# Kernel tuning notes

Hardware: AMD Instinct MI355X
Metric: run time of the kernel (lower is better)

## Reference

```python
import jax, jax.numpy as jnp
import numpy as np

N, E, B, F, D, H, M = 50000, 800000, 1, 64, 64, 4, 8
d = D // H  # head feats = 16


def setup_inputs() -> dict:
    key = jax.random.key(0)
    ks = jax.random.split(key, 16)
    s = 0.02  # init stddev, per reset_parameters
    return {
        "x_src": jax.random.normal(ks[0], (N, B, F), jnp.float32),
        "x_dst": jax.random.normal(ks[1], (N, B, F), jnp.float32),
        "t": jax.random.uniform(ks[2], (N, B, 1), jnp.float32),
        "m": jax.random.uniform(ks[3], (N, 1, M), jnp.float32),
        "ef": jax.random.normal(ks[4], (E, 1), jnp.float32),
        "Wq": s * jax.random.normal(ks[5], (D, F), jnp.float32),
        "Wk": s * jax.random.normal(ks[6], (D, F), jnp.float32),
        "Wv": s * jax.random.normal(ks[7], (D, F), jnp.float32),
        "Wt": s * jax.random.normal(ks[8], (D, F), jnp.float32),
        "We": s * jax.random.normal(ks[9], (D, 1), jnp.float32),
        "Wi": s * jax.random.normal(ks[10], (d * M, d + 1), jnp.float32),
        "bi": jnp.zeros((d * M,), jnp.float32),
        "weight_i": jax.random.normal(ks[11], (M, d), jnp.float32) / np.float32(np.sqrt(d)),
        "scale_i": jnp.zeros((M,), jnp.float32),
        "src": jax.random.randint(ks[12], (E,), 0, N, dtype=jnp.int32),
        "dst": jax.random.randint(ks[13], (E,), 0, N, dtype=jnp.int32),
    }


def reference(x_src, x_dst, t, m, ef, Wq, Wk, Wv, Wt, We, Wi, bi, weight_i, scale_i, src, dst):
    def heads(x, W):  # [N,B,F] -> [N,B,H,d]
        return (x @ W.T).reshape(x.shape[0], B, H, d)

    Q, K = heads(x_dst, Wq), heads(x_src, Wk)
    T, V = heads(x_src, Wt), heads(x_src, Wv)
    Ef = (ef @ We.T).reshape(E, 1, H, d)  # [E,1,H,d], broadcasts over batch

    # --- edge attention scores + edge_softmax over incoming edges of each dst ---
    e = jnp.sum((K[src] + Ef) * Q[dst], axis=-1) / np.float32(np.sqrt(d))  # [E,B,H]
    emax = jax.ops.segment_max(e, dst, num_segments=N)                     # [N,B,H]
    ea = jnp.exp(e - emax[dst])
    ea = ea / jax.ops.segment_sum(ea, dst, num_segments=N)[dst]            # [E,B,H]

    # --- first aggregation: attention-weighted sum of T ---
    g = jax.ops.segment_sum(T[src] * ea[..., None], dst, num_segments=N)   # [N,B,H,d]

    # --- Hawkes mark intensities ---
    tb = jnp.broadcast_to(t[:, :, None, :], (N, B, H, 1))
    u = jax.nn.sigmoid(jnp.concatenate([g, tb], axis=-1) @ Wi.T + bi)      # [N,B,H,M*d]
    u = u.reshape(N, B, H, M, d)
    scale = jnp.exp(scale_i)                                               # [M]
    z = jnp.einsum('nbhmd,md->nbhm', u, weight_i) / scale
    fi = scale * jnp.log1p(jnp.exp(z))                                     # [N,B,H,M]

    # --- intensity-gated second aggregation of V ---
    fm = m[:, :, None, :]                                                  # [N,1,1,M]
    ee = jnp.sum(fi[src] * fm[dst], axis=-1) * ea                          # [E,B,H]
    out = jax.ops.segment_sum(V[src] * ee[..., None], dst, num_segments=N) # [N,B,H,d]
    out = out.reshape(N, B, D)
    return out + x_dst  # residual
```

## Files before the change

### kernel.cpp

```cpp
#include <hip/hip_runtime.h>
#include <cmath>


__device__ __forceinline__ float softplus_f(float z){
  return fmaxf(z, 0.f) + log1pf(__expf(-fabsf(z)));
}

__global__ __launch_bounds__(256) void k_proj(
    const float* __restrict__ x_src, const float* __restrict__ x_dst,
    const float* __restrict__ Wq, const float* __restrict__ Wk,
    const float* __restrict__ Wt, const float* __restrict__ Wv,
    const float* __restrict__ We,
    float* __restrict__ Qo, float* __restrict__ Ko,
    float* __restrict__ To, float* __restrict__ Vo,
    float* __restrict__ WeQ, int N)
{
  __shared__ float sW[4*4096];
  int tid = threadIdx.x;
  {
    float4* dW = (float4*)sW;
    const float4* s0 = (const float4*)Wq;
    const float4* s1 = (const float4*)Wk;
    const float4* s2 = (const float4*)Wt;
    const float4* s3 = (const float4*)Wv;
    #pragma unroll
    for (int i=tid; i<1024; i+=256) dW[i]      = s0[i];
    #pragma unroll
    for (int i=tid; i<1024; i+=256) dW[1024+i] = s1[i];
    #pragma unroll
    for (int i=tid; i<1024; i+=256) dW[2048+i] = s2[i];
    #pragma unroll
    for (int i=tid; i<1024; i+=256) dW[3072+i] = s3[i];
  }
  __syncthreads();

  int l   = tid & 63;
  int mat = __builtin_amdgcn_readfirstlane(tid >> 6);
  int n   = blockIdx.x * 64 + l;
  if (n < N){
    const float* x = ((mat==0) ? x_dst : x_src) + (size_t)n*64;
    float*       O = (mat==0) ? Qo : (mat==1) ? Ko : (mat==2) ? To : Vo;
    const float4* Wm4 = (const float4*)(sW + (mat<<12));
    const float4* We4 = (const float4*)We;

    float xr[64];
    const float4* x4 = (const float4*)x;
    #pragma unroll
    for (int i=0;i<16;i++){ float4 v=x4[i]; xr[4*i]=v.x; xr[4*i+1]=v.y; xr[4*i+2]=v.z; xr[4*i+3]=v.w; }

    float4* O4 = (float4*)(O + (size_t)n*64);
    float weq0=0.f, weq1=0.f, weq2=0.f, weq3=0.f;
    #pragma unroll
    for (int jq=0;jq<16;jq++){
      float a0=0.f,a1=0.f,a2=0.f,a3=0.f;
      const float4* Wr4 = Wm4 + jq*64;
      #pragma unroll
      for (int f4=0;f4<16;f4++){
        float4 w0 = Wr4[f4], w1 = Wr4[16+f4], w2 = Wr4[32+f4], w3 = Wr4[48+f4];
        float x0=xr[4*f4], x1=xr[4*f4+1], x2=xr[4*f4+2], x3=xr[4*f4+3];
        a0=fmaf(w0.x,x0,a0); a0=fmaf(w0.y,x1,a0); a0=fmaf(w0.z,x2,a0); a0=fmaf(w0.w,x3,a0);
        a1=fmaf(w1.x,x0,a1); a1=fmaf(w1.y,x1,a1); a1=fmaf(w1.z,x2,a1); a1=fmaf(w1.w,x3,a1);
        a2=fmaf(w2.x,x0,a2); a2=fmaf(w2.y,x1,a2); a2=fmaf(w2.z,x2,a2); a2=fmaf(w2.w,x3,a2);
        a3=fmaf(w3.x,x0,a3); a3=fmaf(w3.y,x1,a3); a3=fmaf(w3.z,x2,a3); a3=fmaf(w3.w,x3,a3);
      }
      O4[jq] = make_float4(a0,a1,a2,a3);
      if (mat==0){
        float4 we = We4[jq];
        float ws = we.x*a0 + we.y*a1 + we.z*a2 + we.w*a3;
        if      (jq <  4) weq0 += ws;
        else if (jq <  8) weq1 += ws;
        else if (jq < 12) weq2 += ws;
        else              weq3 += ws;
      }
    }
    if (mat==0) *(float4*)(WeQ + (size_t)n*4) = make_float4(weq0,weq1,weq2,weq3);
  }
}

__global__ __launch_bounds__(256) void k_hist(const int* __restrict__ dst, int* __restrict__ deg, int E){
  int i = blockIdx.x*256 + threadIdx.x;
  if (i < E) atomicAdd(&deg[dst[i]], 1);
}

__global__ __launch_bounds__(1024) void k_scan1(const int* __restrict__ deg, int* __restrict__ rowptr,
                                                int* __restrict__ bsum, int N){
  __shared__ int sh[1024];
  int t = threadIdx.x;
  int i = blockIdx.x*1024 + t;
  int v = (i < N) ? deg[i] : 0;
  sh[t] = v; __syncthreads();
  int x = v;
  for (int off=1; off<1024; off<<=1){
    int y = (t >= off) ? sh[t-off] : 0;
    __syncthreads();
    x += y; sh[t] = x;
    __syncthreads();
  }
  if (i < N) rowptr[i] = x - v;
  if (t == 1023) bsum[blockIdx.x] = x;
}

__global__ __launch_bounds__(64) void k_scan2(int* __restrict__ bsum, int nb){
  int l = threadIdx.x;
  int v0 = (l < nb) ? bsum[l] : 0;
  int v = v0;
  for (int off=1; off<64; off<<=1){
    int y = __shfl_up(v, off);
    if (l >= off) v += y;
  }
  if (l < nb) bsum[l] = v - v0;
}

__global__ __launch_bounds__(1024) void k_scan3(int* __restrict__ rowptr, const int* __restrict__ bsum,
                                                int N, int E){
  int i = blockIdx.x*1024 + threadIdx.x;
  if (i < N) rowptr[i] += bsum[blockIdx.x];
  if (i == 0) rowptr[N] = E;
}

__global__ __launch_bounds__(256) void k_scatter(const int* __restrict__ dst, const int* __restrict__ src,
                                                 const float* __restrict__ ef,
                                                 const int* __restrict__ rowptr,
                                                 int* __restrict__ fill,
                                                 int2* __restrict__ sedge, int E){
  int i = blockIdx.x*256 + threadIdx.x;
  if (i < E){
    int d_ = dst[i];
    int pos = rowptr[d_] + atomicAdd(&fill[d_], 1);
    sedge[pos] = make_int2(src[i], __float_as_int(ef[i]));
  }
}

__global__ __launch_bounds__(256) void k_node(
    const float* __restrict__ Qb, const float* __restrict__ Kb, const float* __restrict__ Tb,
    const float* __restrict__ WeQ, const float* __restrict__ t_in,
    const int* __restrict__ rowptr, const int2* __restrict__ sedge,
    const float* __restrict__ Wi, const float* __restrict__ bi,
    const float* __restrict__ wiw, const float* __restrict__ scale_i,
    float* __restrict__ es, float* __restrict__ esum,
    float* __restrict__ fi_out, int N)
{
  __shared__ float sWi[128*17];
  __shared__ float sbi[128];
  __shared__ float swiw[128];
  __shared__ float sscale[8];
  __shared__ float g_sh[4][4][17];
  __shared__ float tr[4][64][9];
  int tid = threadIdx.x;
  for (int i=tid; i<128*17; i+=256) sWi[i] = Wi[i];
  if (tid < 128){ sbi[tid] = bi[tid]; swiw[tid] = wiw[tid]; }
  if (tid < 8)  sscale[tid] = __expf(scale_i[tid]);
  __syncthreads();

  int w = tid>>6, l = tid&63;
  int h = l>>4, e = l&15;
  int n = blockIdx.x*4 + w;
  bool act = (n < N);

  float sacc = 0.f;
  float gacc[16];
  #pragma unroll
  for (int j=0;j<16;j++) gacc[j] = 0.f;
  int dg = 0;

  if (act){
    int row0 = rowptr[n];
    dg = rowptr[n+1] - row0;
    const float4* q4 = (const float4*)(Qb + (size_t)n*64 + (h<<4));
    float q[16];
    #pragma unroll
    for (int j=0;j<4;j++){
      float4 v = q4[j];
      q[4*j]=v.x*0.25f; q[4*j+1]=v.y*0.25f; q[4*j+2]=v.z*0.25f; q[4*j+3]=v.w*0.25f;
    }
    float weq = WeQ[n*4 + h] * 0.25f;

    int2 pv = (dg > 0 && e < dg) ? sedge[row0+e] : make_int2(0,0);
    for (int c0=0; c0<dg; c0+=16){
      int cnt = dg - c0;
      int2 cur = pv;
      if (c0+16 < dg && e < cnt-16) pv = sedge[row0+c0+16+e];
      int sn = cur.x;
      float efv = __int_as_float(cur.y);
      const float4* K4 = (const float4*)(Kb + ((size_t)sn<<6) + (h<<4));
      const float4* T4 = (const float4*)(Tb + ((size_t)sn<<6) + (h<<4));
      float4 k0=K4[0], k1=K4[1], k2=K4[2], k3=K4[3];
      float p0 = fmaf(k0.x,q[0],  fmaf(k0.y,q[1],  fmaf(k0.z,q[2],  k0.w*q[3])));
      float p1 = fmaf(k1.x,q[4],  fmaf(k1.y,q[5],  fmaf(k1.z,q[6],  k1.w*q[7])));
      float p2 = fmaf(k2.x,q[8],  fmaf(k2.y,q[9],  fmaf(k2.z,q[10], k2.w*q[11])));
      float p3 = fmaf(k3.x,q[12], fmaf(k3.y,q[13], fmaf(k3.z,q[14], k3.w*q[15])));
      float dot = (p0+p1)+(p2+p3);
      float p = __expf(fmaf(efv, weq, dot));
      if (e >= cnt) p = 0.f;
      if (e < cnt)  es[(size_t)(row0+c0+e)*4 + h] = p;
      sacc += p;
      float4 t0=T4[0], t1=T4[1], t2=T4[2], t3=T4[3];
      gacc[0] =fmaf(t0.x,p,gacc[0]);  gacc[1] =fmaf(t0.y,p,gacc[1]);
      gacc[2] =fmaf(t0.z,p,gacc[2]);  gacc[3] =fmaf(t0.w,p,gacc[3]);
      gacc[4] =fmaf(t1.x,p,gacc[4]);  gacc[5] =fmaf(t1.y,p,gacc[5]);
      gacc[6] =fmaf(t1.z,p,gacc[6]);  gacc[7] =fmaf(t1.w,p,gacc[7]);
      gacc[8] =fmaf(t2.x,p,gacc[8]);  gacc[9] =fmaf(t2.y,p,gacc[9]);
      gacc[10]=fmaf(t2.z,p,gacc[10]); gacc[11]=fmaf(t2.w,p,gacc[11]);
      gacc[12]=fmaf(t3.x,p,gacc[12]); gacc[13]=fmaf(t3.y,p,gacc[13]);
      gacc[14]=fmaf(t3.z,p,gacc[14]); gacc[15]=fmaf(t3.w,p,gacc[15]);
    }
  }

  sacc += __shfl_xor(sacc,1); sacc += __shfl_xor(sacc,2);
  sacc += __shfl_xor(sacc,4); sacc += __shfl_xor(sacc,8);
  if (act && e == 0) esum[n*4 + h] = sacc;
  float invs = (dg > 0) ? 1.f/sacc : 0.f;

  float gval = 0.f;
  *(float4*)&tr[w][l][0] = make_float4(gacc[0],gacc[1],gacc[2],gacc[3]);
  *(float4*)&tr[w][l][4] = make_float4(gacc[4],gacc[5],gacc[6],gacc[7]);
  if (e < 8){
    float s = 0.f;
    #pragma unroll
    for (int ee=0; ee<16; ee++) s += tr[w][(h<<4)+ee][e];
    gval = s;
  }
  *(float4*)&tr[w][l][0] = make_float4(gacc[8],gacc[9],gacc[10],gacc[11]);
  *(float4*)&tr[w][l][4] = make_float4(gacc[12],gacc[13],gacc[14],gacc[15]);
  if (e >= 8){
    float s = 0.f;
    #pragma unroll
    for (int ee=0; ee<16; ee++) s += tr[w][(h<<4)+ee][e-8];
    gval = s;
  }
  if (act){
    g_sh[w][h][e] = gval * invs;
    if (l < 4) g_sh[w][l][16] = t_in[n];
  }

  if (act){
    float wi1[17], wi2[17];
    #pragma unroll
    for (int j=0;j<17;j++){ wi1[j] = sWi[l*17 + j]; wi2[j] = sWi[(l+64)*17 + j]; }
    float b1 = sbi[l],  b2 = sbi[l+64];
    float wv1 = swiw[l], wv2 = swiw[l+64];
    float z1[4], z2[4];
    #pragma unroll
    for (int h2=0; h2<4; h2++){
      float a1=b1, a2=b2;
      #pragma unroll
      for (int j=0;j<17;j++){
        float inj = g_sh[w][h2][j];
        a1 = fmaf(wi1[j], inj, a1);
        a2 = fmaf(wi2[j], inj, a2);
      }
      float u1 = __fdividef(1.f, 1.f + __expf(-a1));
      float u2 = __fdividef(1.f, 1.f + __expf(-a2));
      float p1 = u1*wv1, p2 = u2*wv2;
      p1 += __shfl_xor(p1,1); p1 += __shfl_xor(p1,2); p1 += __shfl_xor(p1,4); p1 += __shfl_xor(p1,8);
      p2 += __shfl_xor(p2,1); p2 += __shfl_xor(p2,2); p2 += __shfl_xor(p2,4); p2 += __shfl_xor(p2,8);
      z1[h2] = p1; z2[h2] = p2;
    }
    if (e == 0){
      int m1 = h;
      float sc1 = sscale[m1], sc2 = sscale[m1+4];
      #pragma unroll
      for (int h2=0; h2<4; h2++){
        fi_out[(size_t)n*32 + h2*8 + m1    ] = sc1*softplus_f(z1[h2]/sc1);
        fi_out[(size_t)n*32 + h2*8 + m1 + 4] = sc2*softplus_f(z2[h2]/sc2);
      }
    }
  }
}

__global__ __launch_bounds__(256) void k_out(
    const float* __restrict__ Vb, const float* __restrict__ fi,
    const float* __restrict__ es, const float* __restrict__ esum,
    const float* __restrict__ m_in, const float* __restrict__ x_dst,
    const int* __restrict__ rowptr, const int2* __restrict__ sedge,
    float* __restrict__ out, int N)
{
  __shared__ float tr[4][64][9];
  int tid = threadIdx.x;
  int w = tid>>6, l = tid&63;
  int h = l>>4, e = l&15;
  int n = blockIdx.x*4 + w;
  if (n >= N) return;

  float vacc[16];
  #pragma unroll
  for (int j=0;j<16;j++) vacc[j] = 0.f;

  int row0 = rowptr[n];
  int dg = rowptr[n+1] - row0;
  float fm[8];
  const float4* m4 = (const float4*)(m_in + (size_t)n*8);
  float4 fma_=m4[0], fmb_=m4[1];
  fm[0]=fma_.x; fm[1]=fma_.y; fm[2]=fma_.z; fm[3]=fma_.w;
  fm[4]=fmb_.x; fm[5]=fmb_.y; fm[6]=fmb_.z; fm[7]=fmb_.w;
  float sh = esum[n*4 + h];
  float invs = (dg > 0 && sh > 0.f) ? 1.f/sh : 0.f;

  int2 pv = (dg > 0 && e < dg) ? sedge[row0+e] : make_int2(0,0);
  for (int c0=0; c0<dg; c0+=16){
    int cnt = dg - c0;
    int sn = pv.x;
    if (c0+16 < dg && e < cnt-16) pv = sedge[row0+c0+16+e];
    float pe = (e < cnt) ? es[(size_t)(row0+c0+e)*4 + h] : 0.f;
    const float4* F4 = (const float4*)(fi + ((size_t)sn<<5) + (h<<3));
    float4 f0=F4[0], f1=F4[1];
    float dt = fmaf(f0.x,fm[0], fmaf(f0.y,fm[1], fmaf(f0.z,fm[2], fmaf(f0.w,fm[3],
               fmaf(f1.x,fm[4], fmaf(f1.y,fm[5], fmaf(f1.z,fm[6], f1.w*fm[7])))))));
    float wgt = dt * pe;
    const float4* V4 = (const float4*)(Vb + ((size_t)sn<<6) + (h<<4));
    float4 v0=V4[0], v1=V4[1], v2=V4[2], v3=V4[3];
    vacc[0] =fmaf(v0.x,wgt,vacc[0]);  vacc[1] =fmaf(v0.y,wgt,vacc[1]);
    vacc[2] =fmaf(v0.z,wgt,vacc[2]);  vacc[3] =fmaf(v0.w,wgt,vacc[3]);
    vacc[4] =fmaf(v1.x,wgt,vacc[4]);  vacc[5] =fmaf(v1.y,wgt,vacc[5]);
    vacc[6] =fmaf(v1.z,wgt,vacc[6]);  vacc[7] =fmaf(v1.w,wgt,vacc[7]);
    vacc[8] =fmaf(v2.x,wgt,vacc[8]);  vacc[9] =fmaf(v2.y,wgt,vacc[9]);
    vacc[10]=fmaf(v2.z,wgt,vacc[10]); vacc[11]=fmaf(v2.w,wgt,vacc[11]);
    vacc[12]=fmaf(v3.x,wgt,vacc[12]); vacc[13]=fmaf(v3.y,wgt,vacc[13]);
    vacc[14]=fmaf(v3.z,wgt,vacc[14]); vacc[15]=fmaf(v3.w,wgt,vacc[15]);
  }

  float oval = 0.f;
  *(float4*)&tr[w][l][0] = make_float4(vacc[0],vacc[1],vacc[2],vacc[3]);
  *(float4*)&tr[w][l][4] = make_float4(vacc[4],vacc[5],vacc[6],vacc[7]);
  if (e < 8){
    float s = 0.f;
    #pragma unroll
    for (int ee=0; ee<16; ee++) s += tr[w][(h<<4)+ee][e];
    oval = s;
  }
  *(float4*)&tr[w][l][0] = make_float4(vacc[8],vacc[9],vacc[10],vacc[11]);
  *(float4*)&tr[w][l][4] = make_float4(vacc[12],vacc[13],vacc[14],vacc[15]);
  if (e >= 8){
    float s = 0.f;
    #pragma unroll
    for (int ee=0; ee<16; ee++) s += tr[w][(h<<4)+ee][e-8];
    oval = s;
  }
  out[(size_t)n*64 + l] = fmaf(oval, invs, x_dst[(size_t)n*64 + l]);
}

extern "C" void kernel_launch(void* const* d_in, const int* in_sizes, int n_in,
                              void* d_out, int out_size, void* d_ws, size_t ws_size,
                              hipStream_t stream)
{
  const float* x_src = (const float*)d_in[0];
  const float* x_dst = (const float*)d_in[1];
  const float* t_in  = (const float*)d_in[2];
  const float* m_in  = (const float*)d_in[3];
  const float* ef    = (const float*)d_in[4];
  const float* Wq    = (const float*)d_in[5];
  const float* Wk    = (const float*)d_in[6];
  const float* Wv    = (const float*)d_in[7];
  const float* Wt    = (const float*)d_in[8];
  const float* We    = (const float*)d_in[9];
  const float* Wi    = (const float*)d_in[10];
  const float* bi    = (const float*)d_in[11];
  const float* wiw   = (const float*)d_in[12];
  const float* sci   = (const float*)d_in[13];
  const int*   src   = (const int*)d_in[14];
  const int*   dst   = (const int*)d_in[15];
  int N = in_sizes[0] / 64;
  int E = in_sizes[14];
  float* out = (float*)d_out;

  char* p = (char*)d_ws;
  auto alloc = [&](size_t bytes)->char*{ char* r = p; p += (bytes + 255) & ~(size_t)255; return r; };
  float* Qb   = (float*)alloc((size_t)N*64*4);
  float* Kb   = (float*)alloc((size_t)N*64*4);
  float* Tb   = (float*)alloc((size_t)N*64*4);
  float* Vb   = (float*)alloc((size_t)N*64*4);
  float* WeQ  = (float*)alloc((size_t)N*4*4);
  float* esum = (float*)alloc((size_t)N*4*4);
  float* fi   = (float*)alloc((size_t)N*32*4);
  float* es   = (float*)alloc((size_t)E*4*4);
  int*   deg  = (int*)alloc((size_t)N*4);
  int*   fill = (int*)alloc((size_t)N*4);
  int*   rowp = (int*)alloc((size_t)(N+1)*4);
  int2*  sedge= (int2*)alloc((size_t)E*8);
  int    NB   = (N + 1023) / 1024;
  int*   bsum = (int*)alloc((size_t)NB*4);

  hipMemsetAsync(deg,  0, (size_t)N*4, stream);
  hipMemsetAsync(fill, 0, (size_t)N*4, stream);

  k_proj<<<(N+63)/64, 256, 0, stream>>>(x_src, x_dst, Wq, Wk, Wt, Wv, We, Qb, Kb, Tb, Vb, WeQ, N);
  k_hist<<<(E+255)/256, 256, 0, stream>>>(dst, deg, E);
  k_scan1<<<NB, 1024, 0, stream>>>(deg, rowp, bsum, N);
  k_scan2<<<1, 64, 0, stream>>>(bsum, NB);
  k_scan3<<<NB, 1024, 0, stream>>>(rowp, bsum, N, E);
  k_scatter<<<(E+255)/256, 256, 0, stream>>>(dst, src, ef, rowp, fill, sedge, E);
  k_node<<<(N+3)/4, 256, 0, stream>>>(Qb, Kb, Tb, WeQ, t_in, rowp, sedge,
                                      Wi, bi, wiw, sci, es, esum, fi, N);
  k_out<<<(N+3)/4, 256, 0, stream>>>(Vb, fi, es, esum, m_in, x_dst, rowp, sedge, out, N);
}
```

Measured before the change: 375.5 us.

## Store gathered K/T and V/fi node features as interleaved bf16

The projected K and T features are stored as bf16, interleaved per node and head so that one edge gather fetches both from a single contiguous 64-byte segment. V and the mark intensities fi are likewise packed together as bf16 per head. This halves the bytes moved by the random per-edge gathers in the node and output kernels and cuts the number of separate cache lines touched per edge. The cost is reduced precision on K, T, V and fi, which adds rounding error to the attention scores and the aggregated output.

```diff
diff --git a/kernel.cpp b/kernel.cpp
--- a/kernel.cpp
+++ b/kernel.cpp
@@ -5,15 +5,24 @@
 __device__ __forceinline__ float softplus_f(float z){
   return fmaxf(z, 0.f) + log1pf(__expf(-fabsf(z)));
 }
+__device__ __forceinline__ unsigned short f2bf(float x){
+  unsigned int u = __float_as_uint(x);
+  unsigned int r = (u + 0x7fffu + ((u>>16)&1u)) >> 16;
+  return (unsigned short)r;
+}
+__device__ __forceinline__ unsigned int pack2bf(float a, float b){
+  return (unsigned int)f2bf(a) | ((unsigned int)f2bf(b) << 16);
+}
+__device__ __forceinline__ float bflo(unsigned int u){ return __uint_as_float(u << 16); }
+__device__ __forceinline__ float bfhi(unsigned int u){ return __uint_as_float(u & 0xffff0000u); }
 
 __global__ __launch_bounds__(256) void k_proj(
     const float* __restrict__ x_src, const float* __restrict__ x_dst,
     const float* __restrict__ Wq, const float* __restrict__ Wk,
     const float* __restrict__ Wt, const float* __restrict__ Wv,
     const float* __restrict__ We,
-    float* __restrict__ Qo, float* __restrict__ Ko,
-    float* __restrict__ To, float* __restrict__ Vo,
-    float* __restrict__ WeQ, int N)
+    float* __restrict__ Qo, unsigned short* __restrict__ KT16,
+    unsigned short* __restrict__ Vfi16, float* __restrict__ WeQ, int N)
 {
   __shared__ float sW[4*4096];
   int tid = threadIdx.x;
@@ -39,7 +48,6 @@
   int n   = blockIdx.x * 64 + l;
   if (n < N){
     const float* x = ((mat==0) ? x_dst : x_src) + (size_t)n*64;
-    float*       O = (mat==0) ? Qo : (mat==1) ? Ko : (mat==2) ? To : Vo;
     const float4* Wm4 = (const float4*)(sW + (mat<<12));
     const float4* We4 = (const float4*)We;
 
@@ -48,7 +56,7 @@
     #pragma unroll
     for (int i=0;i<16;i++){ float4 v=x4[i]; xr[4*i]=v.x; xr[4*i+1]=v.y; xr[4*i+2]=v.z; xr[4*i+3]=v.w; }
 
-    float4* O4 = (float4*)(O + (size_t)n*64);
+    float4* Q4 = (float4*)(Qo + (size_t)n*64);
     float weq0=0.f, weq1=0.f, weq2=0.f, weq3=0.f;
     #pragma unroll
     for (int jq=0;jq<16;jq++){
@@ -63,14 +71,21 @@
         a2=fmaf(w2.x,x0,a2); a2=fmaf(w2.y,x1,a2); a2=fmaf(w2.z,x2,a2); a2=fmaf(w2.w,x3,a2);
         a3=fmaf(w3.x,x0,a3); a3=fmaf(w3.y,x1,a3); a3=fmaf(w3.z,x2,a3); a3=fmaf(w3.w,x3,a3);
       }
-      O4[jq] = make_float4(a0,a1,a2,a3);
+      int hq = jq>>2, sq = jq&3;
       if (mat==0){
+        Q4[jq] = make_float4(a0,a1,a2,a3);
         float4 we = We4[jq];
         float ws = we.x*a0 + we.y*a1 + we.z*a2 + we.w*a3;
         if      (jq <  4) weq0 += ws;
         else if (jq <  8) weq1 += ws;
         else if (jq < 12) weq2 += ws;
         else              weq3 += ws;
+      } else if (mat==1){
+        *(uint2*)(KT16 + (size_t)n*128 + hq*32 + sq*4) = make_uint2(pack2bf(a0,a1), pack2bf(a2,a3));
+      } else if (mat==2){
+        *(uint2*)(KT16 + (size_t)n*128 + hq*32 + 16 + sq*4) = make_uint2(pack2bf(a0,a1), pack2bf(a2,a3));
+      } else {
+        *(uint2*)(Vfi16 + (size_t)n*96 + hq*24 + sq*4) = make_uint2(pack2bf(a0,a1), pack2bf(a2,a3));
       }
     }
     if (mat==0) *(float4*)(WeQ + (size_t)n*4) = make_float4(weq0,weq1,weq2,weq3);
@@ -132,13 +147,13 @@
 }
 
 __global__ __launch_bounds__(256) void k_node(
-    const float* __restrict__ Qb, const float* __restrict__ Kb, const float* __restrict__ Tb,
+    const float* __restrict__ Qb, const unsigned short* __restrict__ KT16,
     const float* __restrict__ WeQ, const float* __restrict__ t_in,
     const int* __restrict__ rowptr, const int2* __restrict__ sedge,
     const float* __restrict__ Wi, const float* __restrict__ bi,
     const float* __restrict__ wiw, const float* __restrict__ scale_i,
     float* __restrict__ es, float* __restrict__ esum,
-    float* __restrict__ fi_out, int N)
+    unsigned short* __restrict__ Vfi16, int N)
 {
   __shared__ float sWi[128*17];
   __shared__ float sbi[128];
@@ -182,27 +197,30 @@
       if (c0+16 < dg && e < cnt-16) pv = sedge[row0+c0+16+e];
       int sn = cur.x;
       float efv = __int_as_float(cur.y);
-      const float4* K4 = (const float4*)(Kb + ((size_t)sn<<6) + (h<<4));
-      const float4* T4 = (const float4*)(Tb + ((size_t)sn<<6) + (h<<4));
-      float4 k0=K4[0], k1=K4[1], k2=K4[2], k3=K4[3];
-      float p0 = fmaf(k0.x,q[0],  fmaf(k0.y,q[1],  fmaf(k0.z,q[2],  k0.w*q[3])));
-      float p1 = fmaf(k1.x,q[4],  fmaf(k1.y,q[5],  fmaf(k1.z,q[6],  k1.w*q[7])));
-      float p2 = fmaf(k2.x,q[8],  fmaf(k2.y,q[9],  fmaf(k2.z,q[10], k2.w*q[11])));
-      float p3 = fmaf(k3.x,q[12], fmaf(k3.y,q[13], fmaf(k3.z,q[14], k3.w*q[15])));
-      float dot = (p0+p1)+(p2+p3);
-      float p = __expf(fmaf(efv, weq, dot));
+      const uint4* G4 = (const uint4*)(KT16 + ((size_t)sn<<7) + (h<<5));
+      uint4 g0=G4[0], g1=G4[1];
+      uint4 g2=G4[2], g3=G4[3];
+      float d = 0.f;
+      d=fmaf(bflo(g0.x),q[0],d);  d=fmaf(bfhi(g0.x),q[1],d);
+      d=fmaf(bflo(g0.y),q[2],d);  d=fmaf(bfhi(g0.y),q[3],d);
+      d=fmaf(bflo(g0.z),q[4],d);  d=fmaf(bfhi(g0.z),q[5],d);
+      d=fmaf(bflo(g0.w),q[6],d);  d=fmaf(bfhi(g0.w),q[7],d);
+      d=fmaf(bflo(g1.x),q[8],d);  d=fmaf(bfhi(g1.x),q[9],d);
+      d=fmaf(bflo(g1.y),q[10],d); d=fmaf(bfhi(g1.y),q[11],d);
+      d=fmaf(bflo(g1.z),q[12],d); d=fmaf(bfhi(g1.z),q[13],d);
+      d=fmaf(bflo(g1.w),q[14],d); d=fmaf(bfhi(g1.w),q[15],d);
+      float p = __expf(fmaf(efv, weq, d));
       if (e >= cnt) p = 0.f;
       if (e < cnt)  es[(size_t)(row0+c0+e)*4 + h] = p;
       sacc += p;
-      float4 t0=T4[0], t1=T4[1], t2=T4[2], t3=T4[3];
-      gacc[0] =fmaf(t0.x,p,gacc[0]);  gacc[1] =fmaf(t0.y,p,gacc[1]);
-      gacc[2] =fmaf(t0.z,p,gacc[2]);  gacc[3] =fmaf(t0.w,p,gacc[3]);
-      gacc[4] =fmaf(t1.x,p,gacc[4]);  gacc[5] =fmaf(t1.y,p,gacc[5]);
-      gacc[6] =fmaf(t1.z,p,gacc[6]);  gacc[7] =fmaf(t1.w,p,gacc[7]);
-      gacc[8] =fmaf(t2.x,p,gacc[8]);  gacc[9] =fmaf(t2.y,p,gacc[9]);
-      gacc[10]=fmaf(t2.z,p,gacc[10]); gacc[11]=fmaf(t2.w,p,gacc[11]);
-      gacc[12]=fmaf(t3.x,p,gacc[12]); gacc[13]=fmaf(t3.y,p,gacc[13]);
-      gacc[14]=fmaf(t3.z,p,gacc[14]); gacc[15]=fmaf(t3.w,p,gacc[15]);
+      gacc[0] =fmaf(bflo(g2.x),p,gacc[0]);  gacc[1] =fmaf(bfhi(g2.x),p,gacc[1]);
+      gacc[2] =fmaf(bflo(g2.y),p,gacc[2]);  gacc[3] =fmaf(bfhi(g2.y),p,gacc[3]);
+      gacc[4] =fmaf(bflo(g2.z),p,gacc[4]);  gacc[5] =fmaf(bfhi(g2.z),p,gacc[5]);
+      gacc[6] =fmaf(bflo(g2.w),p,gacc[6]);  gacc[7] =fmaf(bfhi(g2.w),p,gacc[7]);
+      gacc[8] =fmaf(bflo(g3.x),p,gacc[8]);  gacc[9] =fmaf(bfhi(g3.x),p,gacc[9]);
+      gacc[10]=fmaf(bflo(g3.y),p,gacc[10]); gacc[11]=fmaf(bfhi(g3.y),p,gacc[11]);
+      gacc[12]=fmaf(bflo(g3.z),p,gacc[12]); gacc[13]=fmaf(bfhi(g3.z),p,gacc[13]);
+      gacc[14]=fmaf(bflo(g3.w),p,gacc[14]); gacc[15]=fmaf(bfhi(g3.w),p,gacc[15]);
     }
   }
 
@@ -261,15 +279,15 @@
       float sc1 = sscale[m1], sc2 = sscale[m1+4];
       #pragma unroll
       for (int h2=0; h2<4; h2++){
-        fi_out[(size_t)n*32 + h2*8 + m1    ] = sc1*softplus_f(z1[h2]/sc1);
-        fi_out[(size_t)n*32 + h2*8 + m1 + 4] = sc2*softplus_f(z2[h2]/sc2);
+        Vfi16[(size_t)n*96 + h2*24 + 16 + m1    ] = f2bf(sc1*softplus_f(z1[h2]/sc1));
+        Vfi16[(size_t)n*96 + h2*24 + 16 + m1 + 4] = f2bf(sc2*softplus_f(z2[h2]/sc2));
       }
     }
   }
 }
 
 __global__ __launch_bounds__(256) void k_out(
-    const float* __restrict__ Vb, const float* __restrict__ fi,
+    const unsigned short* __restrict__ Vfi16,
     const float* __restrict__ es, const float* __restrict__ esum,
     const float* __restrict__ m_in, const float* __restrict__ x_dst,
     const int* __restrict__ rowptr, const int2* __restrict__ sedge,
@@ -302,21 +320,20 @@
     int sn = pv.x;
     if (c0+16 < dg && e < cnt-16) pv = sedge[row0+c0+16+e];
     float pe = (e < cnt) ? es[(size_t)(row0+c0+e)*4 + h] : 0.f;
-    const float4* F4 = (const float4*)(fi + ((size_t)sn<<5) + (h<<3));
-    float4 f0=F4[0], f1=F4[1];
-    float dt = fmaf(f0.x,fm[0], fmaf(f0.y,fm[1], fmaf(f0.z,fm[2], fmaf(f0.w,fm[3],
-               fmaf(f1.x,fm[4], fmaf(f1.y,fm[5], fmaf(f1.z,fm[6], f1.w*fm[7])))))));
+    const uint4* B4 = (const uint4*)(Vfi16 + (size_t)sn*96 + h*24);
+    uint4 b0=B4[0], b1=B4[1];
+    uint4 b2=B4[2];
+    float dt = fmaf(bflo(b2.x),fm[0], fmaf(bfhi(b2.x),fm[1], fmaf(bflo(b2.y),fm[2], fmaf(bfhi(b2.y),fm[3],
+               fmaf(bflo(b2.z),fm[4], fmaf(bfhi(b2.z),fm[5], fmaf(bflo(b2.w),fm[6], bfhi(b2.w)*fm[7])))))));
     float wgt = dt * pe;
-    const float4* V4 = (const float4*)(Vb + ((size_t)sn<<6) + (h<<4));
-    float4 v0=V4[0], v1=V4[1], v2=V4[2], v3=V4[3];
-    vacc[0] =fmaf(v0.x,wgt,vacc[0]);  vacc[1] =fmaf(v0.y,wgt,vacc[1]);
-    vacc[2] =fmaf(v0.z,wgt,vacc[2]);  vacc[3] =fmaf(v0.w,wgt,vacc[3]);
-    vacc[4] =fmaf(v1.x,wgt,vacc[4]);  vacc[5] =fmaf(v1.y,wgt,vacc[5]);
-    vacc[6] =fmaf(v1.z,wgt,vacc[6]);  vacc[7] =fmaf(v1.w,wgt,vacc[7]);
-    vacc[8] =fmaf(v2.x,wgt,vacc[8]);  vacc[9] =fmaf(v2.y,wgt,vacc[9]);
-    vacc[10]=fmaf(v2.z,wgt,vacc[10]); vacc[11]=fmaf(v2.w,wgt,vacc[11]);
-    vacc[12]=fmaf(v3.x,wgt,vacc[12]); vacc[13]=fmaf(v3.y,wgt,vacc[13]);
-    vacc[14]=fmaf(v3.z,wgt,vacc[14]); vacc[15]=fmaf(v3.w,wgt,vacc[15]);
+    vacc[0] =fmaf(bflo(b0.x),wgt,vacc[0]);  vacc[1] =fmaf(bfhi(b0.x),wgt,vacc[1]);
+    vacc[2] =fmaf(bflo(b0.y),wgt,vacc[2]);  vacc[3] =fmaf(bfhi(b0.y),wgt,vacc[3]);
+    vacc[4] =fmaf(bflo(b0.z),wgt,vacc[4]);  vacc[5] =fmaf(bfhi(b0.z),wgt,vacc[5]);
+    vacc[6] =fmaf(bflo(b0.w),wgt,vacc[6]);  vacc[7] =fmaf(bfhi(b0.w),wgt,vacc[7]);
+    vacc[8] =fmaf(bflo(b1.x),wgt,vacc[8]);  vacc[9] =fmaf(bfhi(b1.x),wgt,vacc[9]);
+    vacc[10]=fmaf(bflo(b1.y),wgt,vacc[10]); vacc[11]=fmaf(bfhi(b1.y),wgt,vacc[11]);
+    vacc[12]=fmaf(bflo(b1.z),wgt,vacc[12]); vacc[13]=fmaf(bfhi(b1.z),wgt,vacc[13]);
+    vacc[14]=fmaf(bflo(b1.w),wgt,vacc[14]); vacc[15]=fmaf(bfhi(b1.w),wgt,vacc[15]);
   }
 
   float oval = 0.f;
@@ -365,31 +382,29 @@
 
   char* p = (char*)d_ws;
   auto alloc = [&](size_t bytes)->char*{ char* r = p; p += (bytes + 255) & ~(size_t)255; return r; };
-  float* Qb   = (float*)alloc((size_t)N*64*4);
-  float* Kb   = (float*)alloc((size_t)N*64*4);
-  float* Tb   = (float*)alloc((size_t)N*64*4);
-  float* Vb   = (float*)alloc((size_t)N*64*4);
-  float* WeQ  = (float*)alloc((size_t)N*4*4);
-  float* esum = (float*)alloc((size_t)N*4*4);
-  float* fi   = (float*)alloc((size_t)N*32*4);
-  float* es   = (float*)alloc((size_t)E*4*4);
-  int*   deg  = (int*)alloc((size_t)N*4);
-  int*   fill = (int*)alloc((size_t)N*4);
-  int*   rowp = (int*)alloc((size_t)(N+1)*4);
-  int2*  sedge= (int2*)alloc((size_t)E*8);
-  int    NB   = (N + 1023) / 1024;
-  int*   bsum = (int*)alloc((size_t)NB*4);
+  float*          Qb    = (float*)alloc((size_t)N*64*4);
+  unsigned short* KT16  = (unsigned short*)alloc((size_t)N*128*2);
+  unsigned short* Vfi16 = (unsigned short*)alloc((size_t)N*96*2);
+  float*          WeQ   = (float*)alloc((size_t)N*4*4);
+  float*          esum  = (float*)alloc((size_t)N*4*4);
+  float*          es    = (float*)alloc((size_t)E*4*4);
+  int*            deg   = (int*)alloc((size_t)N*4);
+  int*            fill  = (int*)alloc((size_t)N*4);
+  int*            rowp  = (int*)alloc((size_t)(N+1)*4);
+  int2*           sedge = (int2*)alloc((size_t)E*8);
+  int             NB    = (N + 1023) / 1024;
+  int*            bsum  = (int*)alloc((size_t)NB*4);
 
   hipMemsetAsync(deg,  0, (size_t)N*4, stream);
   hipMemsetAsync(fill, 0, (size_t)N*4, stream);
 
-  k_proj<<<(N+63)/64, 256, 0, stream>>>(x_src, x_dst, Wq, Wk, Wt, Wv, We, Qb, Kb, Tb, Vb, WeQ, N);
+  k_proj<<<(N+63)/64, 256, 0, stream>>>(x_src, x_dst, Wq, Wk, Wt, Wv, We, Qb, KT16, Vfi16, WeQ, N);
   k_hist<<<(E+255)/256, 256, 0, stream>>>(dst, deg, E);
   k_scan1<<<NB, 1024, 0, stream>>>(deg, rowp, bsum, N);
   k_scan2<<<1, 64, 0, stream>>>(bsum, NB);
   k_scan3<<<NB, 1024, 0, stream>>>(rowp, bsum, N, E);
   k_scatter<<<(E+255)/256, 256, 0, stream>>>(dst, src, ef, rowp, fill, sedge, E);
-  k_node<<<(N+3)/4, 256, 0, stream>>>(Qb, Kb, Tb, WeQ, t_in, rowp, sedge,
-                                      Wi, bi, wiw, sci, es, esum, fi, N);
-  k_out<<<(N+3)/4, 256, 0, stream>>>(Vb, fi, es, esum, m_in, x_dst, rowp, sedge, out, N);
-}
+  k_node<<<(N+3)/4, 256, 0, stream>>>(Qb, KT16, WeQ, t_in, rowp, sedge,
+                                      Wi, bi, wiw, sci, es, esum, Vfi16, N);
+  k_out<<<(N+3)/4, 256, 0, stream>>>(Vfi16, es, esum, m_in, x_dst, rowp, sedge, out, N);
+}
```

Measured after the change: 340.2 us, median of 2. 9.4% less time.
